# Kernel tuning notes

Measured on AMD Instinct MI355X. Metric: run time of the kernel, lower is better.

Reference implementation:

```python
import jax, jax.numpy as jnp
import numpy as np

NUM_NODES = 10000
NUM_EDGES = 640000
IN_CH = 128
HID = 128
OUT_CH = 1


def setup_inputs() -> dict:
    key = jax.random.key(0)
    ks = jax.random.split(key, 12)
    x = jax.random.normal(ks[0], (NUM_NODES, IN_CH), dtype=jnp.float32)
    edge_index = jax.random.randint(ks[1], (2, NUM_EDGES), 0, NUM_NODES, dtype=jnp.int64)
    edge_weight = jax.random.uniform(ks[2], (NUM_EDGES,), dtype=jnp.float32)
    s1 = 1.0 / np.sqrt(IN_CH)
    s2 = 1.0 / np.sqrt(HID)
    W1 = jax.random.uniform(ks[3], (HID, IN_CH), minval=-s1, maxval=s1, dtype=jnp.float32)
    b1 = jnp.zeros((HID,), dtype=jnp.float32)
    W2 = jax.random.uniform(ks[4], (HID, HID), minval=-s2, maxval=s2, dtype=jnp.float32)
    b2 = jnp.zeros((HID,), dtype=jnp.float32)
    sc = 1.0 / np.sqrt(HID * 3)
    conv_w = jax.random.uniform(ks[5], (HID, HID, 3), minval=-sc, maxval=sc, dtype=jnp.float32)
    conv_b = jax.random.uniform(ks[6], (HID,), minval=-sc, maxval=sc, dtype=jnp.float32)
    fc_w = jax.random.uniform(ks[7], (OUT_CH, HID), minval=-s2, maxval=s2, dtype=jnp.float32)
    fc_b = jax.random.uniform(ks[8], (OUT_CH,), minval=-s2, maxval=s2, dtype=jnp.float32)
    return {"x": x, "edge_index": edge_index, "edge_weight": edge_weight,
            "W1": W1, "b1": b1, "W2": W2, "b2": b2,
            "conv_w": conv_w, "conv_b": conv_b, "fc_w": fc_w, "fc_b": fc_b}


def _gcn_conv(x, row, col, norm, W, b):
    # PyG GCNConv: linear (no bias in lin), normalized scatter-add, then bias
    xw = x @ W.T                                   # [N, out]
    msg = xw[row] * norm[:, None]                  # gather + edge scale [E, out]
    out = jax.ops.segment_sum(msg, col, num_segments=NUM_NODES)
    return out + b


def reference(x, edge_index, edge_weight, W1, b1, W2, b2, conv_w, conv_b, fc_w, fc_b):
    # gcn_norm with self-loops (fill_value=1.0)
    loop = jnp.arange(NUM_NODES, dtype=edge_index.dtype)
    row = jnp.concatenate([edge_index[0], loop])
    col = jnp.concatenate([edge_index[1], loop])
    w = jnp.concatenate([edge_weight, jnp.ones((NUM_NODES,), dtype=edge_weight.dtype)])
    deg = jax.ops.segment_sum(w, col, num_segments=NUM_NODES)
    dinv = jnp.where(deg > 0, jax.lax.rsqrt(deg), 0.0)
    norm = dinv[row] * w * dinv[col]

    h = jax.nn.relu(_gcn_conv(x, row, col, norm, W1, b1))
    # dropout is identity in eval mode
    h = jax.nn.relu(_gcn_conv(h, row, col, norm, W2, b2))

    # temporal conv1d over node axis: [N,H] -> [1,H,N]
    hc = h.T[None, :, :]
    hc = jax.lax.conv_general_dilated(hc, conv_w, window_strides=(1,),
                                      padding='SAME',
                                      dimension_numbers=('NCH', 'OIH', 'NCH'))
    hc = hc + conv_b[None, :, None]
    h = hc[0].T                                    # [N, H]

    return (h @ fc_w.T + fc_b).squeeze()           # [N]
```

## Files before the change

### kernel.cpp

```cpp
#include <hip/hip_runtime.h>
#include <hip/hip_bf16.h>

#define N_NODES 10000
#define N_EDGES 640000
#define CH 128
#define NB 64
#define EPB (N_EDGES / NB)
#define NCHUNK 40
#define NPAD 10240

__global__ __launch_bounds__(256) void fused_hist_gemm(const int* __restrict__ ei,
        const float* __restrict__ ew,
        const float* __restrict__ x, const float* __restrict__ W1,
        int* __restrict__ hist, float* __restrict__ dhist, int* __restrict__ pcs,
        float* __restrict__ out,
        const float* __restrict__ conv_w, const float* __restrict__ conv_b,
        const float* __restrict__ fc_w, const float* __restrict__ fc_b,
        float* __restrict__ vbuf, float* __restrict__ c0) {
    __shared__ __align__(16) char smem[NPAD * 8];
    int t = threadIdx.x;
    int bid = blockIdx.x;
    if (bid < NB) {
        int* h = (int*)smem;
        float* hf = (float*)(smem + NPAD * 4);
        for (int i = t; i < 2 * NPAD; i += 256) ((int*)smem)[i] = 0;
        __syncthreads();
        int e0 = bid * EPB;
        for (int i = t; i < EPB; i += 256) {
            int e = e0 + i;
            int c = ei[N_EDGES + e];
            atomicAdd(&h[c], 1);
            atomicAdd(&hf[c], ew[e]);
        }
        __syncthreads();
        for (int i = t; i < N_NODES; i += 256) {
            hist[bid * N_NODES + i] = h[i];
            dhist[bid * N_NODES + i] = hf[i];
        }
        int lane = t & 63, wave = t >> 6;
        for (int cch = wave; cch < NCHUNK; cch += 4) {
            int s = h[cch * 256 + lane] + h[cch * 256 + lane + 64]
                  + h[cch * 256 + lane + 128] + h[cch * 256 + lane + 192];
            #pragma unroll
            for (int off = 32; off > 0; off >>= 1) s += __shfl_down(s, off, 64);
            if (lane == 0) pcs[cch * NB + bid] = s;
        }
        return;
    }
    if (bid == NB + (N_NODES + 63) / 64) {
        for (int i = t; i <= 384; i += 256) {
            if (i < 384) {
                float s = 0.0f;
                for (int o = 0; o < CH; ++o) s += fc_w[o] * conv_w[o * 384 + i];
                vbuf[i] = s;
            } else {
                float s = fc_b[0];
                for (int o = 0; o < CH; ++o) s += fc_w[o] * conv_b[o];
                *c0 = s;
            }
        }
        return;
    }
    float (*As)[68]  = (float(*)[68])smem;
    float (*Ws)[132] = (float(*)[132])(smem + 32 * 68 * sizeof(float));
    int tx = t & 31;
    int ty = t >> 5;
    int row0 = (bid - NB) * 64;
    float acc[8][4] = {};
    for (int k0 = 0; k0 < 128; k0 += 32) {
        #pragma unroll
        for (int i = 0; i < 8; ++i) {
            int idx = t + i * 256;
            int r = idx >> 5, k = idx & 31;
            int gr = row0 + r;
            As[k][r] = (gr < N_NODES) ? x[gr * CH + k0 + k] : 0.0f;
        }
        #pragma unroll
        for (int i = 0; i < 16; ++i) {
            int idx = t + i * 256;
            int o = idx >> 5, k = idx & 31;
            Ws[k][o] = W1[o * CH + k0 + k];
        }
        __syncthreads();
        #pragma unroll
        for (int kk = 0; kk < 32; ++kk) {
            float a[8], w[4];
            #pragma unroll
            for (int j = 0; j < 8; ++j) a[j] = As[kk][ty * 8 + j];
            #pragma unroll
            for (int c = 0; c < 4; ++c) w[c] = Ws[kk][tx * 4 + c];
            #pragma unroll
            for (int j = 0; j < 8; ++j)
                #pragma unroll
                for (int c = 0; c < 4; ++c)
                    acc[j][c] += a[j] * w[c];
        }
        __syncthreads();
    }
    #pragma unroll
    for (int j = 0; j < 8; ++j) {
        int gr = row0 + ty * 8 + j;
        if (gr < N_NODES) {
            float4 v = make_float4(acc[j][0], acc[j][1], acc[j][2], acc[j][3]);
            *reinterpret_cast<float4*>(&out[gr * CH + tx * 4]) = v;
        }
    }
}

__global__ __launch_bounds__(256) void bofs_kernel(int* __restrict__ hist,
        const float* __restrict__ dhist, const int* __restrict__ pcs,
        int* __restrict__ tot, int* __restrict__ offs, float* __restrict__ dinv) {
    __shared__ int wred[4];
    __shared__ int wsum[4];
    __shared__ int base_sh;
    int blk = blockIdx.x, t = threadIdx.x;
    int lane = t & 63, wave = t >> 6;
    int bsum = 0;
    for (int i = t; i < blk * NB; i += 256) bsum += pcs[i];
    #pragma unroll
    for (int off = 32; off > 0; off >>= 1) bsum += __shfl_down(bsum, off, 64);
    if (lane == 0) wred[wave] = bsum;
    __syncthreads();
    if (t == 0) base_sh = wred[0] + wred[1] + wred[2] + wred[3];
    int n = blk * 256 + t;
    int v = 0;
    if (n < N_NODES) {
        float dsum = 0.0f;
        #pragma unroll 8
        for (int b = 0; b < NB; ++b) {
            v += hist[b * N_NODES + n];
            dsum += dhist[b * N_NODES + n];
        }
        tot[n] = v;
        dinv[n] = rsqrtf(dsum + 1.0f);
    }
    int s = v;
    #pragma unroll
    for (int off = 1; off < 64; off <<= 1) {
        int u = __shfl_up(s, off, 64);
        if (lane >= off) s += u;
    }
    if (lane == 63) wsum[wave] = s;
    __syncthreads();
    int wbase = 0;
    for (int i = 0; i < wave; ++i) wbase += wsum[i];
    if (n < N_NODES) {
        int run = base_sh + wbase + s - v;
        offs[n] = run;
        for (int b = 0; b < NB; ++b) {
            int h = hist[b * N_NODES + n];
            hist[b * N_NODES + n] = run;
            run += h;
        }
    }
}

__global__ __launch_bounds__(256) void scatter_kernel(const int* __restrict__ ei,
        const float* __restrict__ ew, const float* __restrict__ dinv,
        const int* __restrict__ bofs, int2* __restrict__ erec) {
    __shared__ int cur[N_NODES];
    __shared__ float di[N_NODES];
    int b = blockIdx.x, t = threadIdx.x;
    for (int i = t; i < N_NODES; i += 256) {
        cur[i] = bofs[b * N_NODES + i];
        di[i] = dinv[i];
    }
    __syncthreads();
    int e0 = b * EPB;
    for (int i = t; i < EPB; i += 256) {
        int e = e0 + i;
        int r = ei[e];
        int c = ei[N_EDGES + e];
        float v = di[r] * ew[e] * di[c];
        int p = atomicAdd(&cur[c], 1);
        erec[p] = make_int2(r, __float_as_int(v));
    }
}

__global__ __launch_bounds__(256) void agg_gemm_kernel(const float4* __restrict__ xw4,
        const int2* __restrict__ erec, const int* __restrict__ offs,
        const int* __restrict__ cnt, const float* __restrict__ dinv,
        const float4* __restrict__ bias4, const float* __restrict__ W2,
        float* __restrict__ out) {
    __shared__ float hs[8][128];
    int l = threadIdx.x & 31;
    int g = threadIdx.x >> 5;
    int n = blockIdx.x * 8 + g;
    float d = dinv[n];
    float dd = d * d;
    float4 self = xw4[n * 32 + l];
    float4 acc = make_float4(dd * self.x, dd * self.y, dd * self.z, dd * self.w);
    int start = offs[n];
    int num = cnt[n];
    int i = 0;
    for (; i + 8 <= num; i += 8) {
        int2 r[8];
        #pragma unroll
        for (int j = 0; j < 8; ++j) r[j] = erec[start + i + j];
        float4 f[8];
        #pragma unroll
        for (int j = 0; j < 8; ++j) f[j] = xw4[r[j].x * 32 + l];
        #pragma unroll
        for (int j = 0; j < 8; ++j) {
            float v = __int_as_float(r[j].y);
            acc.x += v * f[j].x; acc.y += v * f[j].y;
            acc.z += v * f[j].z; acc.w += v * f[j].w;
        }
    }
    for (; i < num; ++i) {
        int2 r = erec[start + i];
        float4 f = xw4[r.x * 32 + l];
        float v = __int_as_float(r.y);
        acc.x += v * f.x; acc.y += v * f.y; acc.z += v * f.z; acc.w += v * f.w;
    }
    float4 bb = bias4[l];
    acc.x = fmaxf(acc.x + bb.x, 0.0f);
    acc.y = fmaxf(acc.y + bb.y, 0.0f);
    acc.z = fmaxf(acc.z + bb.z, 0.0f);
    acc.w = fmaxf(acc.w + bb.w, 0.0f);
    *reinterpret_cast<float4*>(&hs[g][4 * l]) = acc;
    __syncthreads();
    int o = threadIdx.x & 127;
    int rg = threadIdx.x >> 7;
    const float4* w4p = reinterpret_cast<const float4*>(&W2[o * CH]);
    const float4* h0p = reinterpret_cast<const float4*>(&hs[rg * 4 + 0][0]);
    const float4* h1p = reinterpret_cast<const float4*>(&hs[rg * 4 + 1][0]);
    const float4* h2p = reinterpret_cast<const float4*>(&hs[rg * 4 + 2][0]);
    const float4* h3p = reinterpret_cast<const float4*>(&hs[rg * 4 + 3][0]);
    float a0 = 0.0f, a1 = 0.0f, a2 = 0.0f, a3 = 0.0f;
    #pragma unroll 8
    for (int k4 = 0; k4 < 32; ++k4) {
        float4 w = w4p[k4];
        float4 h0 = h0p[k4], h1 = h1p[k4], h2 = h2p[k4], h3 = h3p[k4];
        a0 += w.x * h0.x + w.y * h0.y + w.z * h0.z + w.w * h0.w;
        a1 += w.x * h1.x + w.y * h1.y + w.z * h1.z + w.w * h1.w;
        a2 += w.x * h2.x + w.y * h2.y + w.z * h2.z + w.w * h2.w;
        a3 += w.x * h3.x + w.y * h3.y + w.z * h3.z + w.w * h3.w;
    }
    int nb = blockIdx.x * 8 + rg * 4;
    out[(nb + 0) * CH + o] = a0;
    out[(nb + 1) * CH + o] = a1;
    out[(nb + 2) * CH + o] = a2;
    out[(nb + 3) * CH + o] = a3;
}

__global__ __launch_bounds__(256) void agg_kernel(const float4* __restrict__ xw4,
        const int2* __restrict__ erec, const int* __restrict__ offs,
        const int* __restrict__ cnt, const float* __restrict__ dinv,
        const float4* __restrict__ bias4, float4* __restrict__ out4) {
    int l = threadIdx.x & 31;
    int g = threadIdx.x >> 5;
    int n = blockIdx.x * 8 + g;
    float d = dinv[n];
    float dd = d * d;
    float4 self = xw4[n * 32 + l];
    float4 acc = make_float4(dd * self.x, dd * self.y, dd * self.z, dd * self.w);
    int start = offs[n];
    int num = cnt[n];
    int i = 0;
    for (; i + 8 <= num; i += 8) {
        int2 r[8];
        #pragma unroll
        for (int j = 0; j < 8; ++j) r[j] = erec[start + i + j];
        float4 f[8];
        #pragma unroll
        for (int j = 0; j < 8; ++j) f[j] = xw4[r[j].x * 32 + l];
        #pragma unroll
        for (int j = 0; j < 8; ++j) {
            float v = __int_as_float(r[j].y);
            acc.x += v * f[j].x; acc.y += v * f[j].y;
            acc.z += v * f[j].z; acc.w += v * f[j].w;
        }
    }
    for (; i < num; ++i) {
        int2 r = erec[start + i];
        float4 f = xw4[r.x * 32 + l];
        float v = __int_as_float(r.y);
        acc.x += v * f.x; acc.y += v * f.y; acc.z += v * f.z; acc.w += v * f.w;
    }
    float4 bb = bias4[l];
    acc.x = fmaxf(acc.x + bb.x, 0.0f);
    acc.y = fmaxf(acc.y + bb.y, 0.0f);
    acc.z = fmaxf(acc.z + bb.z, 0.0f);
    acc.w = fmaxf(acc.w + bb.w, 0.0f);
    out4[n * 32 + l] = acc;
}

__global__ __launch_bounds__(256) void convfc_kernel(const float* __restrict__ h,
        const float* __restrict__ v, const float* __restrict__ c0,
        float* __restrict__ out, int N) {
    int n = blockIdx.x * 4 + (threadIdx.x >> 6);
    int l = threadIdx.x & 63;
    if (n >= N) return;
    const float* hn = h + n * CH;
    float v0a = v[l * 3 + 0],        v1a = v[l * 3 + 1],        v2a = v[l * 3 + 2];
    float v0b = v[(l + 64) * 3 + 0], v1b = v[(l + 64) * 3 + 1], v2b = v[(l + 64) * 3 + 2];
    float p = hn[l] * v1a + hn[l + 64] * v1b;
    if (n > 0)     p += hn[l - CH] * v0a + hn[l + 64 - CH] * v0b;
    if (n < N - 1) p += hn[l + CH] * v2a + hn[l + 64 + CH] * v2b;
    #pragma unroll
    for (int off = 32; off > 0; off >>= 1) p += __shfl_down(p, off, 64);
    if (l == 0) out[n] = p + *c0;
}

extern "C" void kernel_launch(void* const* d_in, const int* in_sizes, int n_in,
                              void* d_out, int out_size, void* d_ws, size_t ws_size,
                              hipStream_t stream) {
    const float* x       = (const float*)d_in[0];
    const int*   ei      = (const int*)d_in[1];
    const float* ew      = (const float*)d_in[2];
    const float* W1      = (const float*)d_in[3];
    const float* b1      = (const float*)d_in[4];
    const float* W2      = (const float*)d_in[5];
    const float* b2      = (const float*)d_in[6];
    const float* conv_w  = (const float*)d_in[7];
    const float* conv_b  = (const float*)d_in[8];
    const float* fc_w    = (const float*)d_in[9];
    const float* fc_b    = (const float*)d_in[10];
    float* out = (float*)d_out;

    float* bufA   = (float*)d_ws;
    float* bufB   = bufA + N_NODES * CH;
    int2*  erec   = (int2*)(bufB + N_NODES * CH);
    int*   hist   = (int*)(erec + N_EDGES);
    float* dhist  = (float*)(hist + NB * N_NODES);
    int*   pcs    = (int*)(dhist + NB * N_NODES);
    int*   tot    = pcs + NCHUNK * NB;
    int*   offs   = tot + N_NODES;
    float* dinv   = (float*)(offs + N_NODES);
    float* vbuf   = dinv + N_NODES;
    float* c0     = vbuf + 384;

    const int gemm_grid = (N_NODES + 63) / 64;

    fused_hist_gemm<<<NB + gemm_grid + 1, 256, 0, stream>>>(ei, ew, x, W1,
            hist, dhist, pcs, bufA, conv_w, conv_b, fc_w, fc_b, vbuf, c0);
    bofs_kernel<<<NCHUNK, 256, 0, stream>>>(hist, dhist, pcs, tot, offs, dinv);
    scatter_kernel<<<NB, 256, 0, stream>>>(ei, ew, dinv, hist, erec);
    agg_gemm_kernel<<<N_NODES / 8, 256, 0, stream>>>((const float4*)bufA, erec, offs,
            tot, dinv, (const float4*)b1, W2, bufB);
    agg_kernel<<<N_NODES / 8, 256, 0, stream>>>((const float4*)bufB, erec, offs, tot,
                                                dinv, (const float4*)b2, (float4*)bufA);
    convfc_kernel<<<(N_NODES + 3) / 4, 256, 0, stream>>>(bufA, vbuf, c0, out, N_NODES);
}
```

Baseline: 207.3 us.

## Split second aggregation into two channel-half passes and deepen gather unroll

The second GCN aggregation is split into two launches, each gathering half of the 128 channels as float2 per lane, so each pass touches a smaller slice of the feature table that may fit in cache. Both aggregation kernels also gain a 16-edge unrolled gather loop to keep more loads in flight. The cost is reading the edge records twice, an extra launch, narrower per-lane loads, and higher register use from the larger unroll.

After: 225.7 us. +8.9%, slower.

```diff
diff --git a/kernel.cpp b/kernel.cpp
--- a/kernel.cpp
+++ b/kernel.cpp
@@ -193,6 +193,20 @@
     int start = offs[n];
     int num = cnt[n];
     int i = 0;
+    for (; i + 16 <= num; i += 16) {
+        int2 r[16];
+        #pragma unroll
+        for (int j = 0; j < 16; ++j) r[j] = erec[start + i + j];
+        float4 f[16];
+        #pragma unroll
+        for (int j = 0; j < 16; ++j) f[j] = xw4[r[j].x * 32 + l];
+        #pragma unroll
+        for (int j = 0; j < 16; ++j) {
+            float v = __int_as_float(r[j].y);
+            acc.x += v * f[j].x; acc.y += v * f[j].y;
+            acc.z += v * f[j].z; acc.w += v * f[j].w;
+        }
+    }
     for (; i + 8 <= num; i += 8) {
         int2 r[8];
         #pragma unroll
@@ -244,46 +258,45 @@
     out[(nb + 3) * CH + o] = a3;
 }
 
-__global__ __launch_bounds__(256) void agg_kernel(const float4* __restrict__ xw4,
+__global__ __launch_bounds__(256) void agg_half_kernel(const float* __restrict__ xw,
         const int2* __restrict__ erec, const int* __restrict__ offs,
         const int* __restrict__ cnt, const float* __restrict__ dinv,
-        const float4* __restrict__ bias4, float4* __restrict__ out4) {
+        const float* __restrict__ bias, float* __restrict__ out, int half) {
     int l = threadIdx.x & 31;
     int g = threadIdx.x >> 5;
     int n = blockIdx.x * 8 + g;
+    int cidx = half * 32 + l;
+    const float2* xw2 = (const float2*)xw;
     float d = dinv[n];
     float dd = d * d;
-    float4 self = xw4[n * 32 + l];
-    float4 acc = make_float4(dd * self.x, dd * self.y, dd * self.z, dd * self.w);
+    float2 self = xw2[n * 64 + cidx];
+    float2 acc = make_float2(dd * self.x, dd * self.y);
     int start = offs[n];
     int num = cnt[n];
     int i = 0;
-    for (; i + 8 <= num; i += 8) {
-        int2 r[8];
-        #pragma unroll
-        for (int j = 0; j < 8; ++j) r[j] = erec[start + i + j];
-        float4 f[8];
-        #pragma unroll
-        for (int j = 0; j < 8; ++j) f[j] = xw4[r[j].x * 32 + l];
-        #pragma unroll
-        for (int j = 0; j < 8; ++j) {
+    for (; i + 16 <= num; i += 16) {
+        int2 r[16];
+        #pragma unroll
+        for (int j = 0; j < 16; ++j) r[j] = erec[start + i + j];
+        float2 f[16];
+        #pragma unroll
+        for (int j = 0; j < 16; ++j) f[j] = xw2[r[j].x * 64 + cidx];
+        #pragma unroll
+        for (int j = 0; j < 16; ++j) {
             float v = __int_as_float(r[j].y);
             acc.x += v * f[j].x; acc.y += v * f[j].y;
-            acc.z += v * f[j].z; acc.w += v * f[j].w;
         }
     }
     for (; i < num; ++i) {
         int2 r = erec[start + i];
-        float4 f = xw4[r.x * 32 + l];
+        float2 f = xw2[r.x * 64 + cidx];
         float v = __int_as_float(r.y);
-        acc.x += v * f.x; acc.y += v * f.y; acc.z += v * f.z; acc.w += v * f.w;
-    }
-    float4 bb = bias4[l];
+        acc.x += v * f.x; acc.y += v * f.y;
+    }
+    float2 bb = ((const float2*)bias)[cidx];
     acc.x = fmaxf(acc.x + bb.x, 0.0f);
     acc.y = fmaxf(acc.y + bb.y, 0.0f);
-    acc.z = fmaxf(acc.z + bb.z, 0.0f);
-    acc.w = fmaxf(acc.w + bb.w, 0.0f);
-    out4[n * 32 + l] = acc;
+    ((float2*)out)[n * 64 + cidx] = acc;
 }
 
 __global__ __launch_bounds__(256) void convfc_kernel(const float* __restrict__ h,
@@ -339,7 +352,9 @@
     scatter_kernel<<<NB, 256, 0, stream>>>(ei, ew, dinv, hist, erec);
     agg_gemm_kernel<<<N_NODES / 8, 256, 0, stream>>>((const float4*)bufA, erec, offs,
             tot, dinv, (const float4*)b1, W2, bufB);
-    agg_kernel<<<N_NODES / 8, 256, 0, stream>>>((const float4*)bufB, erec, offs, tot,
-                                                dinv, (const float4*)b2, (float4*)bufA);
+    agg_half_kernel<<<N_NODES / 8, 256, 0, stream>>>(bufB, erec, offs, tot,
+                                                     dinv, b2, bufA, 0);
+    agg_half_kernel<<<N_NODES / 8, 256, 0, stream>>>(bufB, erec, offs, tot,
+                                                     dinv, b2, bufA, 1);
     convfc_kernel<<<(N_NODES + 3) / 4, 256, 0, stream>>>(bufA, vbuf, c0, out, N_NODES);
 }
```

## Regroup each node's edge records by source-row bucket before aggregation

Applied to the files above, without the earlier changes.

Adds a regroup kernel that, within each destination node's CSR segment, reorders edge records into four buckets by source row (row>>11). This aims to improve L2 locality of feature gathers in both aggregation passes, since concurrently running blocks hit similar row ranges of the feature matrix. It costs an extra kernel launch, another full pass over the 640K edge records, and a second edge buffer in workspace. Order within each bucket is set by atomics and is not deterministic.

Result: no change. 211.4 us (+2.0%).

```diff
diff --git a/kernel.cpp b/kernel.cpp
--- a/kernel.cpp
+++ b/kernel.cpp
@@ -177,6 +177,43 @@
     }
 }
 
+__global__ __launch_bounds__(256) void regroup_kernel(const int2* __restrict__ erec,
+        const int* __restrict__ offs, const int* __restrict__ cnt,
+        int2* __restrict__ erec2) {
+    __shared__ int curs[8][5];
+    int g = threadIdx.x >> 5;
+    int l = threadIdx.x & 31;
+    int n = blockIdx.x * 8 + g;
+    int start = offs[n];
+    int num = cnt[n];
+    int c0 = 0, c1 = 0, c2 = 0, c3 = 0;
+    for (int i = l; i < num; i += 32) {
+        int tl = erec[start + i].x >> 11;
+        c0 += (tl == 0); c1 += (tl == 1); c2 += (tl == 2); c3 += (tl == 3);
+    }
+    #pragma unroll
+    for (int off = 16; off > 0; off >>= 1) {
+        c0 += __shfl_down(c0, off, 32);
+        c1 += __shfl_down(c1, off, 32);
+        c2 += __shfl_down(c2, off, 32);
+        c3 += __shfl_down(c3, off, 32);
+    }
+    if (l == 0) {
+        curs[g][0] = start;
+        curs[g][1] = start + c0;
+        curs[g][2] = start + c0 + c1;
+        curs[g][3] = start + c0 + c1 + c2;
+        curs[g][4] = start + c0 + c1 + c2 + c3;
+    }
+    __syncthreads();
+    for (int i = l; i < num; i += 32) {
+        int2 rec = erec[start + i];
+        int tl = rec.x >> 11;
+        int p = atomicAdd(&curs[g][tl], 1);
+        erec2[p] = rec;
+    }
+}
+
 __global__ __launch_bounds__(256) void agg_gemm_kernel(const float4* __restrict__ xw4,
         const int2* __restrict__ erec, const int* __restrict__ offs,
         const int* __restrict__ cnt, const float* __restrict__ dinv,
@@ -322,7 +359,8 @@
     float* bufA   = (float*)d_ws;
     float* bufB   = bufA + N_NODES * CH;
     int2*  erec   = (int2*)(bufB + N_NODES * CH);
-    int*   hist   = (int*)(erec + N_EDGES);
+    int2*  erec2  = erec + N_EDGES;
+    int*   hist   = (int*)(erec2 + N_EDGES);
     float* dhist  = (float*)(hist + NB * N_NODES);
     int*   pcs    = (int*)(dhist + NB * N_NODES);
     int*   tot    = pcs + NCHUNK * NB;
@@ -337,9 +375,10 @@
             hist, dhist, pcs, bufA, conv_w, conv_b, fc_w, fc_b, vbuf, c0);
     bofs_kernel<<<NCHUNK, 256, 0, stream>>>(hist, dhist, pcs, tot, offs, dinv);
     scatter_kernel<<<NB, 256, 0, stream>>>(ei, ew, dinv, hist, erec);
-    agg_gemm_kernel<<<N_NODES / 8, 256, 0, stream>>>((const float4*)bufA, erec, offs,
+    regroup_kernel<<<N_NODES / 8, 256, 0, stream>>>(erec, offs, tot, erec2);
+    agg_gemm_kernel<<<N_NODES / 8, 256, 0, stream>>>((const float4*)bufA, erec2, offs,
             tot, dinv, (const float4*)b1, W2, bufB);
-    agg_kernel<<<N_NODES / 8, 256, 0, stream>>>((const float4*)bufB, erec, offs, tot,
+    agg_kernel<<<N_NODES / 8, 256, 0, stream>>>((const float4*)bufB, erec2, offs, tot,
                                                 dinv, (const float4*)b2, (float4*)bufA);
     convfc_kernel<<<(N_NODES + 3) / 4, 256, 0, stream>>>(bufA, vbuf, c0, out, N_NODES);
 }
```

## Split first GEMM across hist and bofs kernels; shuffle-broadcast edge records in agg

Applied to the files above, without the earlier changes.

The first-layer GEMM is split in two. 78 row tiles now run alongside the histogram blocks and the other 79 tiles run alongside the prefix-offset blocks, so the small bofs stage is overlapped with useful work. The bofs loops are manually unrolled by four to expose more independent loads. agg_kernel gains a 32-edge path in which each lane loads one edge record and the record is broadcast with shuffles, which cuts redundant erec loads. The extra GEMM blocks in bofs_gemm_kernel use a smaller shared-memory footprint, but the hist kernel's larger allocation may limit occupancy for its own GEMM blocks.

After: 217.3 us. +4.9%, slower.

```diff
diff --git a/kernel.cpp b/kernel.cpp
--- a/kernel.cpp
+++ b/kernel.cpp
@@ -8,15 +8,62 @@
 #define EPB (N_EDGES / NB)
 #define NCHUNK 40
 #define NPAD 10240
-
-__global__ __launch_bounds__(256) void fused_hist_gemm(const int* __restrict__ ei,
-        const float* __restrict__ ew,
-        const float* __restrict__ x, const float* __restrict__ W1,
-        int* __restrict__ hist, float* __restrict__ dhist, int* __restrict__ pcs,
-        float* __restrict__ out,
-        const float* __restrict__ conv_w, const float* __restrict__ conv_b,
-        const float* __restrict__ fc_w, const float* __restrict__ fc_b,
-        float* __restrict__ vbuf, float* __restrict__ c0) {
+#define G1A 78
+#define G1B 79
+
+__device__ __forceinline__ void gemm128_body(const float* __restrict__ A,
+        const float* __restrict__ W, float* __restrict__ out, int row0,
+        char* smem) {
+    float (*As)[68]  = (float(*)[68])smem;
+    float (*Ws)[132] = (float(*)[132])(smem + 32 * 68 * sizeof(float));
+    int t = threadIdx.x;
+    int tx = t & 31;
+    int ty = t >> 5;
+    float acc[8][4] = {};
+    for (int k0 = 0; k0 < 128; k0 += 32) {
+        #pragma unroll
+        for (int i = 0; i < 8; ++i) {
+            int idx = t + i * 256;
+            int r = idx >> 5, k = idx & 31;
+            int gr = row0 + r;
+            As[k][r] = (gr < N_NODES) ? A[gr * CH + k0 + k] : 0.0f;
+        }
+        #pragma unroll
+        for (int i = 0; i < 16; ++i) {
+            int idx = t + i * 256;
+            int o = idx >> 5, k = idx & 31;
+            Ws[k][o] = W[o * CH + k0 + k];
+        }
+        __syncthreads();
+        #pragma unroll
+        for (int kk = 0; kk < 32; ++kk) {
+            float a[8], w[4];
+            #pragma unroll
+            for (int j = 0; j < 8; ++j) a[j] = As[kk][ty * 8 + j];
+            #pragma unroll
+            for (int c = 0; c < 4; ++c) w[c] = Ws[kk][tx * 4 + c];
+            #pragma unroll
+            for (int j = 0; j < 8; ++j)
+                #pragma unroll
+                for (int c = 0; c < 4; ++c)
+                    acc[j][c] += a[j] * w[c];
+        }
+        __syncthreads();
+    }
+    #pragma unroll
+    for (int j = 0; j < 8; ++j) {
+        int gr = row0 + ty * 8 + j;
+        if (gr < N_NODES) {
+            float4 v = make_float4(acc[j][0], acc[j][1], acc[j][2], acc[j][3]);
+            *reinterpret_cast<float4*>(&out[gr * CH + tx * 4]) = v;
+        }
+    }
+}
+
+__global__ __launch_bounds__(256) void hist_gemm_kernel(const int* __restrict__ ei,
+        const float* __restrict__ ew, const float* __restrict__ x,
+        const float* __restrict__ W1, int* __restrict__ hist,
+        float* __restrict__ dhist, int* __restrict__ pcs, float* __restrict__ out) {
     __shared__ __align__(16) char smem[NPAD * 8];
     int t = threadIdx.x;
     int bid = blockIdx.x;
@@ -47,7 +94,78 @@
         }
         return;
     }
-    if (bid == NB + (N_NODES + 63) / 64) {
+    gemm128_body(x, W1, out, (bid - NB) * 64, smem);
+}
+
+__global__ __launch_bounds__(256) void bofs_gemm_kernel(int* __restrict__ hist,
+        const float* __restrict__ dhist, const int* __restrict__ pcs,
+        int* __restrict__ tot, int* __restrict__ offs, float* __restrict__ dinv,
+        const float* __restrict__ x, const float* __restrict__ W1,
+        float* __restrict__ out,
+        const float* __restrict__ conv_w, const float* __restrict__ conv_b,
+        const float* __restrict__ fc_w, const float* __restrict__ fc_b,
+        float* __restrict__ vbuf, float* __restrict__ c0) {
+    __shared__ __align__(16) char smem[32 * 68 * 4 + 32 * 132 * 4];
+    int bid = blockIdx.x, t = threadIdx.x;
+    if (bid < NCHUNK) {
+        int* wred = (int*)smem;
+        int* wsum = (int*)smem + 4;
+        int* base_sh = (int*)smem + 8;
+        int lane = t & 63, wave = t >> 6;
+        int bsum = 0;
+        for (int i = t; i < bid * NB; i += 256) bsum += pcs[i];
+        #pragma unroll
+        for (int off = 32; off > 0; off >>= 1) bsum += __shfl_down(bsum, off, 64);
+        if (lane == 0) wred[wave] = bsum;
+        __syncthreads();
+        if (t == 0) *base_sh = wred[0] + wred[1] + wred[2] + wred[3];
+        int n = bid * 256 + t;
+        int v = 0;
+        if (n < N_NODES) {
+            float dsum = 0.0f;
+            for (int b = 0; b < NB; b += 4) {
+                int a0 = hist[(b + 0) * N_NODES + n];
+                int a1 = hist[(b + 1) * N_NODES + n];
+                int a2 = hist[(b + 2) * N_NODES + n];
+                int a3 = hist[(b + 3) * N_NODES + n];
+                float f0 = dhist[(b + 0) * N_NODES + n];
+                float f1 = dhist[(b + 1) * N_NODES + n];
+                float f2 = dhist[(b + 2) * N_NODES + n];
+                float f3 = dhist[(b + 3) * N_NODES + n];
+                v += a0 + a1 + a2 + a3;
+                dsum += f0 + f1 + f2 + f3;
+            }
+            tot[n] = v;
+            dinv[n] = rsqrtf(dsum + 1.0f);
+        }
+        int s = v;
+        #pragma unroll
+        for (int off = 1; off < 64; off <<= 1) {
+            int u = __shfl_up(s, off, 64);
+            if (lane >= off) s += u;
+        }
+        if (lane == 63) wsum[wave] = s;
+        __syncthreads();
+        int wbase = 0;
+        for (int i = 0; i < wave; ++i) wbase += wsum[i];
+        if (n < N_NODES) {
+            int run = *base_sh + wbase + s - v;
+            offs[n] = run;
+            for (int b = 0; b < NB; b += 4) {
+                int h0 = hist[(b + 0) * N_NODES + n];
+                int h1 = hist[(b + 1) * N_NODES + n];
+                int h2 = hist[(b + 2) * N_NODES + n];
+                int h3 = hist[(b + 3) * N_NODES + n];
+                hist[(b + 0) * N_NODES + n] = run;
+                hist[(b + 1) * N_NODES + n] = run + h0;
+                hist[(b + 2) * N_NODES + n] = run + h0 + h1;
+                hist[(b + 3) * N_NODES + n] = run + h0 + h1 + h2;
+                run += h0 + h1 + h2 + h3;
+            }
+        }
+        return;
+    }
+    if (bid == NCHUNK + G1B) {
         for (int i = t; i <= 384; i += 256) {
             if (i < 384) {
                 float s = 0.0f;
@@ -61,98 +179,7 @@
         }
         return;
     }
-    float (*As)[68]  = (float(*)[68])smem;
-    float (*Ws)[132] = (float(*)[132])(smem + 32 * 68 * sizeof(float));
-    int tx = t & 31;
-    int ty = t >> 5;
-    int row0 = (bid - NB) * 64;
-    float acc[8][4] = {};
-    for (int k0 = 0; k0 < 128; k0 += 32) {
-        #pragma unroll
-        for (int i = 0; i < 8; ++i) {
-            int idx = t + i * 256;
-            int r = idx >> 5, k = idx & 31;
-            int gr = row0 + r;
-            As[k][r] = (gr < N_NODES) ? x[gr * CH + k0 + k] : 0.0f;
-        }
-        #pragma unroll
-        for (int i = 0; i < 16; ++i) {
-            int idx = t + i * 256;
-            int o = idx >> 5, k = idx & 31;
-            Ws[k][o] = W1[o * CH + k0 + k];
-        }
-        __syncthreads();
-        #pragma unroll
-        for (int kk = 0; kk < 32; ++kk) {
-            float a[8], w[4];
-            #pragma unroll
-            for (int j = 0; j < 8; ++j) a[j] = As[kk][ty * 8 + j];
-            #pragma unroll
-            for (int c = 0; c < 4; ++c) w[c] = Ws[kk][tx * 4 + c];
-            #pragma unroll
-            for (int j = 0; j < 8; ++j)
-                #pragma unroll
-                for (int c = 0; c < 4; ++c)
-                    acc[j][c] += a[j] * w[c];
-        }
-        __syncthreads();
-    }
-    #pragma unroll
-    for (int j = 0; j < 8; ++j) {
-        int gr = row0 + ty * 8 + j;
-        if (gr < N_NODES) {
-            float4 v = make_float4(acc[j][0], acc[j][1], acc[j][2], acc[j][3]);
-            *reinterpret_cast<float4*>(&out[gr * CH + tx * 4]) = v;
-        }
-    }
-}
-
-__global__ __launch_bounds__(256) void bofs_kernel(int* __restrict__ hist,
-        const float* __restrict__ dhist, const int* __restrict__ pcs,
-        int* __restrict__ tot, int* __restrict__ offs, float* __restrict__ dinv) {
-    __shared__ int wred[4];
-    __shared__ int wsum[4];
-    __shared__ int base_sh;
-    int blk = blockIdx.x, t = threadIdx.x;
-    int lane = t & 63, wave = t >> 6;
-    int bsum = 0;
-    for (int i = t; i < blk * NB; i += 256) bsum += pcs[i];
-    #pragma unroll
-    for (int off = 32; off > 0; off >>= 1) bsum += __shfl_down(bsum, off, 64);
-    if (lane == 0) wred[wave] = bsum;
-    __syncthreads();
-    if (t == 0) base_sh = wred[0] + wred[1] + wred[2] + wred[3];
-    int n = blk * 256 + t;
-    int v = 0;
-    if (n < N_NODES) {
-        float dsum = 0.0f;
-        #pragma unroll 8
-        for (int b = 0; b < NB; ++b) {
-            v += hist[b * N_NODES + n];
-            dsum += dhist[b * N_NODES + n];
-        }
-        tot[n] = v;
-        dinv[n] = rsqrtf(dsum + 1.0f);
-    }
-    int s = v;
-    #pragma unroll
-    for (int off = 1; off < 64; off <<= 1) {
-        int u = __shfl_up(s, off, 64);
-        if (lane >= off) s += u;
-    }
-    if (lane == 63) wsum[wave] = s;
-    __syncthreads();
-    int wbase = 0;
-    for (int i = 0; i < wave; ++i) wbase += wsum[i];
-    if (n < N_NODES) {
-        int run = base_sh + wbase + s - v;
-        offs[n] = run;
-        for (int b = 0; b < NB; ++b) {
-            int h = hist[b * N_NODES + n];
-            hist[b * N_NODES + n] = run;
-            run += h;
-        }
-    }
+    gemm128_body(x, W1, out, 4992 + (bid - NCHUNK) * 64, smem);
 }
 
 __global__ __launch_bounds__(256) void scatter_kernel(const int* __restrict__ ei,
@@ -258,6 +285,27 @@
     int start = offs[n];
     int num = cnt[n];
     int i = 0;
+    for (; i + 32 <= num; i += 32) {
+        int2 my = erec[start + i + l];
+        float myv = __int_as_float(my.y);
+        #pragma unroll
+        for (int jb = 0; jb < 32; jb += 8) {
+            int rx[8]; float rv[8];
+            #pragma unroll
+            for (int k = 0; k < 8; ++k) {
+                rx[k] = __shfl(my.x, jb + k, 32);
+                rv[k] = __shfl(myv,  jb + k, 32);
+            }
+            float4 f[8];
+            #pragma unroll
+            for (int k = 0; k < 8; ++k) f[k] = xw4[rx[k] * 32 + l];
+            #pragma unroll
+            for (int k = 0; k < 8; ++k) {
+                acc.x += rv[k] * f[k].x; acc.y += rv[k] * f[k].y;
+                acc.z += rv[k] * f[k].z; acc.w += rv[k] * f[k].w;
+            }
+        }
+    }
     for (; i + 8 <= num; i += 8) {
         int2 r[8];
         #pragma unroll
@@ -331,11 +379,10 @@
     float* vbuf   = dinv + N_NODES;
     float* c0     = vbuf + 384;
 
-    const int gemm_grid = (N_NODES + 63) / 64;
-
-    fused_hist_gemm<<<NB + gemm_grid + 1, 256, 0, stream>>>(ei, ew, x, W1,
-            hist, dhist, pcs, bufA, conv_w, conv_b, fc_w, fc_b, vbuf, c0);
-    bofs_kernel<<<NCHUNK, 256, 0, stream>>>(hist, dhist, pcs, tot, offs, dinv);
+    hist_gemm_kernel<<<NB + G1A, 256, 0, stream>>>(ei, ew, x, W1, hist, dhist,
+                                                   pcs, bufA);
+    bofs_gemm_kernel<<<NCHUNK + G1B + 1, 256, 0, stream>>>(hist, dhist, pcs, tot,
+            offs, dinv, x, W1, bufA, conv_w, conv_b, fc_w, fc_b, vbuf, c0);
     scatter_kernel<<<NB, 256, 0, stream>>>(ei, ew, dinv, hist, erec);
     agg_gemm_kernel<<<N_NODES / 8, 256, 0, stream>>>((const float4*)bufA, erec, offs,
             tot, dinv, (const float4*)b1, W2, bufB);
```
